# Kernel optimization log

Hardware: AMD Instinct MI355X
Metric: run time of the kernel (lower is better)

## Reference

```python
import jax, jax.numpy as jnp
import numpy as np

N, E, G = 100000, 800000, 4096
H, F_NODE, F_EDGE, T_OUT = 256, 133, 7, 12
NUM_LAYERS, NUM_TIMESTEPS = 4, 2
SLOPE = 0.01  # negative_slope used throughout AttentiveFP


def _lrelu(v):
    return jax.nn.leaky_relu(v, SLOPE)


def _seg_softmax(logits, seg, n):
    # PyG softmax: exp(x - segment_max) / (segment_sum + 1e-16)
    m = jax.ops.segment_max(logits, seg, num_segments=n)
    e = jnp.exp(logits - m[seg])
    s = jax.ops.segment_sum(e, seg, num_segments=n)
    return e / (s[seg] + 1e-16)


def _gru(xin, h, w_ih, w_hh, b_ih, b_hh):
    # torch.nn.GRUCell, gate order (r, z, n)
    gi = xin @ w_ih.T + b_ih
    gh = h @ w_hh.T + b_hh
    i_r, i_z, i_n = jnp.split(gi, 3, axis=-1)
    h_r, h_z, h_n = jnp.split(gh, 3, axis=-1)
    r = jax.nn.sigmoid(i_r + h_r)
    z = jax.nn.sigmoid(i_z + h_z)
    n = jnp.tanh(i_n + r * h_n)
    return (1.0 - z) * n + z * h


def setup_inputs() -> dict:
    key = jax.random.key(0)
    ks = iter(jax.random.split(key, 40))
    rn = lambda shape, s=0.1: jax.random.normal(next(ks), shape, jnp.float32) * s
    return {
        'x': jax.random.normal(next(ks), (N, F_NODE), jnp.float32),
        'edge_attr': jax.random.normal(next(ks), (E, F_EDGE), jnp.float32),
        'lin1_w': rn((H, F_NODE)), 'lin1_b': rn((H,)),
        'gate_att_l': rn((H,)), 'gate_att_r': rn((H,)),
        'gate_lin1_w': rn((H, H + F_EDGE)), 'gate_lin2_w': rn((H, H)), 'gate_bias': rn((H,)),
        'atom_lin_w': rn((NUM_LAYERS - 1, H, H)), 'atom_att_src': rn((NUM_LAYERS - 1, H)),
        'atom_att_dst': rn((NUM_LAYERS - 1, H)), 'atom_bias': rn((NUM_LAYERS - 1, H)),
        'gru_w_ih': rn((NUM_LAYERS, 3 * H, H)), 'gru_w_hh': rn((NUM_LAYERS, 3 * H, H)),
        'gru_b_ih': rn((NUM_LAYERS, 3 * H)), 'gru_b_hh': rn((NUM_LAYERS, 3 * H)),
        'mol_lin_w': rn((H, H)), 'mol_att_src': rn((H,)), 'mol_att_dst': rn((H,)), 'mol_bias': rn((H,)),
        'mol_gru_w_ih': rn((3 * H, H)), 'mol_gru_w_hh': rn((3 * H, H)),
        'mol_gru_b_ih': rn((3 * H,)), 'mol_gru_b_hh': rn((3 * H,)),
        'lin2_w': rn((H, H)), 'lin2_b': rn((H,)),
        'fc_w': rn((T_OUT, H)), 'fc_b': rn((T_OUT,)),
        'edge_index': jax.random.randint(next(ks), (2, E), 0, N),
        'batch': jnp.sort(jax.random.randint(next(ks), (N,), 0, G)),
        'num_graphs': G,
    }


def reference(x, edge_attr, lin1_w, lin1_b, gate_att_l, gate_att_r, gate_lin1_w,
              gate_lin2_w, gate_bias, atom_lin_w, atom_att_src, atom_att_dst, atom_bias,
              gru_w_ih, gru_w_hh, gru_b_ih, gru_b_hh, mol_lin_w, mol_att_src, mol_att_dst,
              mol_bias, mol_gru_w_ih, mol_gru_w_hh, mol_gru_b_ih, mol_gru_b_hh,
              lin2_w, lin2_b, fc_w, fc_b, edge_index, batch, num_graphs):
    # Eval mode: all dropouts are identity.
    src, dst = edge_index[0], edge_index[1]
    n = x.shape[0]

    x0 = _lrelu(x @ lin1_w.T + lin1_b)  # [N, H]

    # --- GATEConv: edge-feature attention message passing ---
    xj = _lrelu(jnp.concatenate([x0[src], edge_attr], axis=-1) @ gate_lin1_w.T)  # [E, H]
    alpha = _lrelu(xj @ gate_att_l + (x0 @ gate_att_r)[dst])
    alpha = _seg_softmax(alpha, dst, n)
    msg = (x0 @ gate_lin2_w.T)[src] * alpha[:, None]  # [E, H]
    h = jax.ops.segment_sum(msg, dst, num_segments=n) + gate_bias
    xcur = jax.nn.relu(_gru(jax.nn.elu(h), x0, gru_w_ih[0], gru_w_hh[0], gru_b_ih[0], gru_b_hh[0]))

    # --- (num_layers-1) GATConv layers (heads=1, no self loops, slope 0.01) ---
    for l in range(atom_lin_w.shape[0]):
        xl = xcur @ atom_lin_w[l].T  # [N, H]
        a = _lrelu((xl @ atom_att_src[l])[src] + (xl @ atom_att_dst[l])[dst])
        a = _seg_softmax(a, dst, n)
        h = jax.ops.segment_sum(xl[src] * a[:, None], dst, num_segments=n) + atom_bias[l]
        xcur = jax.nn.relu(_gru(jax.nn.elu(h), xcur,
                                gru_w_ih[l + 1], gru_w_hh[l + 1], gru_b_ih[l + 1], gru_b_hh[l + 1]))

    # --- Molecule embedding: attention pooling over node->graph bipartite edges ---
    out = jax.nn.relu(jax.ops.segment_sum(xcur, batch, num_segments=num_graphs))  # [G, H]
    xm = xcur @ mol_lin_w.T              # src transform, fixed across timesteps
    a_src = xm @ mol_att_src             # [N]
    for _ in range(NUM_TIMESTEPS):
        a = _lrelu(a_src + ((out @ mol_lin_w.T) @ mol_att_dst)[batch])
        a = _seg_softmax(a, batch, num_graphs)
        h = jax.ops.segment_sum(xm * a[:, None], batch, num_segments=num_graphs) + mol_bias
        out = jax.nn.relu(_gru(jax.nn.elu(h), out,
                               mol_gru_w_ih, mol_gru_w_hh, mol_gru_b_ih, mol_gru_b_hh))

    emb = out @ lin2_w.T + lin2_b        # AttentiveFP lin2
    return emb @ fc_w.T + fc_b           # [G, num_tasks]
```

## Files before the change

### kernel.cpp

```cpp
#include <hip/hip_runtime.h>
#include <math.h>
#include <stdio.h>
#include <stdint.h>

#define NH 256
#define NH3 768
#define FNODE 133
#define FEDGE 7
#define LDW_GATE1 263
#define NGRAPH 4096
#define NTASK 12
#define SLOPE 0.01f
#define CHUNK 25000
#define PADK 40
#define KPAD_X 160
#define LDC2 512
#define SCAN_TILE 2048

typedef __attribute__((ext_vector_type(4))) float f32x4;
typedef __attribute__((ext_vector_type(8))) _Float16 f16x8;
typedef __attribute__((ext_vector_type(4))) _Float16 f16x4;
typedef __attribute__((ext_vector_type(2))) _Float16 f16x2;

static __device__ __forceinline__ float lrelu_f(float x) { return x > 0.f ? x : SLOPE * x; }
static __device__ __forceinline__ f16x2 lrelu2(f16x2 v) {
    f16x2 z = {(_Float16)0.f, (_Float16)0.f};
    f16x2 s = {(_Float16)SLOPE, (_Float16)SLOPE};
    return __builtin_elementwise_max(v, z) + __builtin_elementwise_min(v, z) * s;
}

template<int ACT>
static __device__ __forceinline__ void gemm16_core(
    _Float16* As, _Float16* Ws,
    const _Float16* __restrict__ A, const _Float16* __restrict__ Wf,
    const float* __restrict__ bias, const float* __restrict__ bias2,
    _Float16* __restrict__ Cout,
    int M, int K, int ldA, int ldC, int ocol)
{
    const int bm = blockIdx.y * 64;
    const int tid = threadIdx.x;
    const int wv = tid >> 6, lane = tid & 63;
    const int l15 = lane & 15, l4 = lane >> 4;
    const int ar = tid >> 2, akq = (tid & 3) * 8;
    const int ga = bm + ar;

    f16x8 ra, rw[4];
    auto loadT = [&](int k0) {
        if (ga < M) ra = *reinterpret_cast<const f16x8*>(A + (size_t)ga * ldA + k0 + akq);
        else { f16x8 z = {}; ra = z; }
#pragma unroll
        for (int q = 0; q < 4; ++q)
            rw[q] = *reinterpret_cast<const f16x8*>(Wf + (size_t)(ar + 64 * q) * K + k0 + akq);
    };

    f32x4 acc[16];
#pragma unroll
    for (int c = 0; c < 16; ++c) acc[c] = (f32x4){0.f, 0.f, 0.f, 0.f};

    loadT(0);
    for (int k0 = 0; k0 < K; k0 += 32) {
        *reinterpret_cast<f16x8*>(&As[ar * PADK + akq]) = ra;
#pragma unroll
        for (int q = 0; q < 4; ++q)
            *reinterpret_cast<f16x8*>(&Ws[(ar + 64 * q) * PADK + akq]) = rw[q];
        __syncthreads();
        if (k0 + 32 < K) loadT(k0 + 32);
        f16x8 af = *reinterpret_cast<const f16x8*>(&As[(wv * 16 + l15) * PADK + l4 * 8]);
#pragma unroll
        for (int c = 0; c < 16; ++c) {
            f16x8 wf = *reinterpret_cast<const f16x8*>(&Ws[(c * 16 + l15) * PADK + l4 * 8]);
            acc[c] = __builtin_amdgcn_mfma_f32_16x16x32_f16(af, wf, acc[c], 0, 0, 0);
        }
        __syncthreads();
    }

#pragma unroll
    for (int c = 0; c < 16; ++c) {
        int gc = c * 16 + l15;
        float bv = (bias ? bias[gc] : 0.f) + (bias2 ? bias2[gc] : 0.f);
#pragma unroll
        for (int q = 0; q < 4; ++q) {
            int gr = bm + wv * 16 + l4 * 4 + q;
            if (gr >= M) continue;
            float v = acc[c][q] + bv;
            if (ACT == 1) v = lrelu_f(v);
            else if (ACT == 2) v = (v > 0.f ? v : expm1f(v));
            else if (ACT == 3) v = 1.f / (1.f + expf(-v));
            Cout[(size_t)gr * ldC + ocol + gc] = (_Float16)v;
        }
    }
}

template<int ACT>
__global__ __launch_bounds__(256, 4) void gemm16(
    const _Float16* __restrict__ A, const _Float16* __restrict__ Wf,
    const float* __restrict__ bias, _Float16* __restrict__ Cout,
    int M, int K, int ldA, int ldC, int ocol)
{
    __shared__ _Float16 As[64 * PADK];
    __shared__ _Float16 Ws[256 * PADK];
    gemm16_core<ACT>(As, Ws, A, Wf, bias, nullptr, Cout, M, K, ldA, ldC, ocol);
}

__global__ __launch_bounds__(256, 4) void gemm_gru_a16(
    const _Float16* __restrict__ Acat, const _Float16* __restrict__ wcat16,
    const _Float16* __restrict__ wihn16,
    const float* __restrict__ bih, const float* __restrict__ bhh,
    _Float16* __restrict__ srz, _Float16* __restrict__ innb, int mc)
{
    __shared__ _Float16 As[64 * PADK];
    __shared__ _Float16 Ws[256 * PADK];
    int z = blockIdx.z;
    if (z < 2)
        gemm16_core<3>(As, Ws, Acat, wcat16 + (size_t)z * 256 * 512, bih + z * 256, bhh + z * 256,
                       srz, mc, 512, LDC2, 512, z * 256);
    else
        gemm16_core<0>(As, Ws, Acat, wihn16, bih + 512, nullptr, innb, mc, 256, LDC2, 256, 0);
}

__global__ __launch_bounds__(256, 4) void gemm_gru_b16(
    _Float16* __restrict__ Acat, const _Float16* __restrict__ Wn16, const float* __restrict__ bhh,
    const _Float16* __restrict__ srz, const _Float16* __restrict__ innb,
    const float* __restrict__ us, const float* __restrict__ ud,
    float* __restrict__ dotr, float* __restrict__ adst, int mc)
{
    __shared__ _Float16 As[64 * PADK];
    __shared__ _Float16 Ws[256 * PADK];
    const int bm = blockIdx.y * 64;
    const int tid = threadIdx.x;
    const int wv = tid >> 6, lane = tid & 63;
    const int l15 = lane & 15, l4 = lane >> 4;
    const int ar = tid >> 2, akq = (tid & 3) * 8;
    const int ga = bm + ar;

    f16x8 ra, rw[4];
    auto loadT = [&](int k0) {
        if (ga < mc) ra = *reinterpret_cast<const f16x8*>(Acat + (size_t)ga * LDC2 + NH + k0 + akq);
        else { f16x8 z = {}; ra = z; }
#pragma unroll
        for (int q = 0; q < 4; ++q)
            rw[q] = *reinterpret_cast<const f16x8*>(Wn16 + (size_t)(ar + 64 * q) * NH + k0 + akq);
    };

    f32x4 acc[16];
#pragma unroll
    for (int c = 0; c < 16; ++c) acc[c] = (f32x4){0.f, 0.f, 0.f, 0.f};

    loadT(0);
    for (int k0 = 0; k0 < NH; k0 += 32) {
        *reinterpret_cast<f16x8*>(&As[ar * PADK + akq]) = ra;
#pragma unroll
        for (int q = 0; q < 4; ++q)
            *reinterpret_cast<f16x8*>(&Ws[(ar + 64 * q) * PADK + akq]) = rw[q];
        __syncthreads();
        if (k0 + 32 < NH) loadT(k0 + 32);
        f16x8 af = *reinterpret_cast<const f16x8*>(&As[(wv * 16 + l15) * PADK + l4 * 8]);
#pragma unroll
        for (int c = 0; c < 16; ++c) {
            f16x8 wf = *reinterpret_cast<const f16x8*>(&Ws[(c * 16 + l15) * PADK + l4 * 8]);
            acc[c] = __builtin_amdgcn_mfma_f32_16x16x32_f16(af, wf, acc[c], 0, 0, 0);
        }
        __syncthreads();
    }

    float pd1[4] = {0.f, 0.f, 0.f, 0.f};
    float pd2[4] = {0.f, 0.f, 0.f, 0.f};
#pragma unroll
    for (int c = 0; c < 16; ++c) {
        int gc = c * 16 + l15;
        float bhn = bhh[512 + gc];
        float usv = us ? us[gc] : 0.f;
        float udv = ud ? ud[gc] : 0.f;
#pragma unroll
        for (int q = 0; q < 4; ++q) {
            int gr = bm + wv * 16 + l4 * 4 + q;
            if (gr >= mc) continue;
            float hn = acc[c][q] + bhn;
            float rr = (float)srz[(size_t)gr * 512 + gc];
            float zz = (float)srz[(size_t)gr * 512 + 256 + gc];
            float inn = (float)innb[(size_t)gr * NH + gc];
            float nn = tanhf(inn + rr * hn);
            size_t xoff = (size_t)gr * LDC2 + NH + gc;
            float xold = (float)Acat[xoff];
            float hv = fmaxf((1.f - zz) * nn + zz * xold, 0.f);
            Acat[xoff] = (_Float16)hv;
            pd1[q] += hv * usv;
            pd2[q] += hv * udv;
        }
    }
    if (us) {
#pragma unroll
        for (int off = 1; off < 16; off <<= 1) {
#pragma unroll
            for (int q = 0; q < 4; ++q) {
                pd1[q] += __shfl_xor(pd1[q], off);
                pd2[q] += __shfl_xor(pd2[q], off);
            }
        }
        if (l15 == 0) {
#pragma unroll
            for (int q = 0; q < 4; ++q) {
                int gr = bm + wv * 16 + l4 * 4 + q;
                if (gr < mc) {
                    dotr[gr] = pd1[q];
                    if (ud) adst[gr] = pd2[q];
                }
            }
        }
    }
}

template<int ACT, int OB, int AF16>
static __device__ __forceinline__ void gemm_core(
    _Float16* As, _Float16* Ws,
    const void* __restrict__ Av, const float* __restrict__ W,
    const float* __restrict__ bias, void* __restrict__ Cout,
    int M, int K, int Nout, int ldA, int ldW, int ldC, int ocol, int Kw, int bn)
{
    const int bm = blockIdx.y * 64;
    const int tid = threadIdx.x;
    const int wv = tid >> 6, lane = tid & 63;
    const int l15 = lane & 15, l4 = lane >> 4;
    const bool kvec = ((K & 31) == 0) && ((ldA & 3) == 0);
    const bool wvec = ((K & 31) == 0) && ((ldW & 3) == 0) && (Kw == K);
    const int ar = tid >> 2, akq = (tid & 3) * 8;

    f32x4 acc[16];
#pragma unroll
    for (int c = 0; c < 16; ++c) acc[c] = (f32x4){0.f, 0.f, 0.f, 0.f};

    for (int k0 = 0; k0 < K; k0 += 32) {
        {
            const int ga = bm + ar;
            _Float16* dstA = &As[ar * PADK + akq];
            if (AF16) {
                const _Float16* A = (const _Float16*)Av;
                if (ga < M) {
                    *reinterpret_cast<f16x8*>(dstA) =
                        *reinterpret_cast<const f16x8*>(A + (size_t)ga * ldA + k0 + akq);
                } else {
#pragma unroll
                    for (int j = 0; j < 8; ++j) dstA[j] = (_Float16)0.f;
                }
            } else {
                const float* A = (const float*)Av;
                if (ga < M && kvec) {
                    const float4* ap4 = reinterpret_cast<const float4*>(A + (size_t)ga * ldA + k0 + akq);
                    float4 v0 = ap4[0], v1 = ap4[1];
                    dstA[0] = (_Float16)v0.x; dstA[1] = (_Float16)v0.y;
                    dstA[2] = (_Float16)v0.z; dstA[3] = (_Float16)v0.w;
                    dstA[4] = (_Float16)v1.x; dstA[5] = (_Float16)v1.y;
                    dstA[6] = (_Float16)v1.z; dstA[7] = (_Float16)v1.w;
                } else {
                    const float* ap = A + (size_t)ga * ldA + k0 + akq;
#pragma unroll
                    for (int j = 0; j < 8; ++j) {
                        int gk = k0 + akq + j;
                        float v = (ga < M && gk < K) ? ap[j] : 0.f;
                        dstA[j] = (_Float16)v;
                    }
                }
            }
        }
#pragma unroll
        for (int q = 0; q < 4; ++q) {
            const int r = ar + 64 * q;
            const int gw = bn + r;
            _Float16* dstW = &Ws[r * PADK + akq];
            if (gw < Nout && wvec) {
                const float4* wp4 = reinterpret_cast<const float4*>(W + (size_t)gw * ldW + k0 + akq);
                float4 v0 = wp4[0], v1 = wp4[1];
                dstW[0] = (_Float16)v0.x; dstW[1] = (_Float16)v0.y;
                dstW[2] = (_Float16)v0.z; dstW[3] = (_Float16)v0.w;
                dstW[4] = (_Float16)v1.x; dstW[5] = (_Float16)v1.y;
                dstW[6] = (_Float16)v1.z; dstW[7] = (_Float16)v1.w;
            } else {
                const float* wp = W + (size_t)gw * ldW + k0 + akq;
#pragma unroll
                for (int j = 0; j < 8; ++j) {
                    int gk = k0 + akq + j;
                    float v = (gw < Nout && gk < Kw) ? wp[j] : 0.f;
                    dstW[j] = (_Float16)v;
                }
            }
        }
        __syncthreads();
        f16x8 af = *reinterpret_cast<const f16x8*>(&As[(wv * 16 + l15) * PADK + l4 * 8]);
#pragma unroll
        for (int c = 0; c < 16; ++c) {
            f16x8 wf = *reinterpret_cast<const f16x8*>(&Ws[(c * 16 + l15) * PADK + l4 * 8]);
            acc[c] = __builtin_amdgcn_mfma_f32_16x16x32_f16(af, wf, acc[c], 0, 0, 0);
        }
        __syncthreads();
    }

#pragma unroll
    for (int c = 0; c < 16; ++c) {
        int gc = bn + c * 16 + l15;
        if (gc >= Nout) continue;
        float bv = bias ? bias[gc] : 0.f;
#pragma unroll
        for (int q = 0; q < 4; ++q) {
            int gr = bm + wv * 16 + l4 * 4 + q;
            if (gr >= M) continue;
            float v = acc[c][q] + bv;
            if (ACT == 1) v = lrelu_f(v);
            else if (ACT == 2) v = (v > 0.f ? v : expm1f(v));
            size_t off = (size_t)gr * ldC + ocol + gc;
            if (OB) ((_Float16*)Cout)[off] = (_Float16)v;
            else    ((float*)Cout)[off] = v;
        }
    }
}

template<int ACT, int OB, int AF16>
__global__ __launch_bounds__(256, 4) void gemm_mfma(
    const void* __restrict__ A, const float* __restrict__ W,
    const float* __restrict__ bias, void* __restrict__ Cout,
    int M, int K, int Nout, int ldA, int ldW, int ldC, int ocol, int Kw)
{
    __shared__ _Float16 As[64 * PADK];
    __shared__ _Float16 Ws[256 * PADK];
    gemm_core<ACT, OB, AF16>(As, Ws, A, W, bias, Cout, M, K, Nout, ldA, ldW, ldC, ocol, Kw,
                             blockIdx.x * 256);
}

template<int ACT, int OB>
__global__ __launch_bounds__(256, 4) void gemm_mfma2(
    const float* __restrict__ A0, const float* __restrict__ A1,
    const float* __restrict__ W0, const float* __restrict__ W1,
    void* __restrict__ C0, void* __restrict__ C1, int M, int K, int Nout)
{
    __shared__ _Float16 As[64 * PADK];
    __shared__ _Float16 Ws[256 * PADK];
    int bn = blockIdx.x * 256;
    if (blockIdx.z == 0)
        gemm_core<ACT, OB, 0>(As, Ws, A0, W0, nullptr, C0, M, K, Nout, K, K, Nout, 0, K, bn);
    else
        gemm_core<ACT, OB, 0>(As, Ws, A1, W1, nullptr, C1, M, K, Nout, K, K, Nout, 0, K, bn);
}

__global__ void cast_w16(const float* __restrict__ src, _Float16* __restrict__ dst,
                         int rows, int cols, int ldsrc, int kout)
{
    int i = blockIdx.x * 256 + threadIdx.x;
    if (i >= rows * kout) return;
    int r = i / kout, k = i % kout;
    dst[i] = (k < cols) ? (_Float16)src[(size_t)r * ldsrc + k] : (_Float16)0.f;
}
__global__ void build_wcat16(const float* __restrict__ wih, const float* __restrict__ whh,
                             _Float16* __restrict__ dst)
{
    int i = blockIdx.x * 256 + threadIdx.x;
    if (i >= 512 * 512) return;
    int j = i >> 9, k = i & 511;
    dst[i] = (_Float16)((k < 256) ? wih[j * 256 + k] : whh[j * 256 + (k - 256)]);
}

__global__ void pad_cast_f16(const float* __restrict__ in, _Float16* __restrict__ out,
                             int M, int Kin, int Kout)
{
    size_t i = (size_t)blockIdx.x * 256 + threadIdx.x;
    if (i >= (size_t)M * Kout) return;
    int r = (int)(i / Kout), k = (int)(i % Kout);
    out[i] = (k < Kin) ? (_Float16)in[(size_t)r * Kin + k] : (_Float16)0.f;
}

__global__ __launch_bounds__(256) void gemm_nt(
    const float* __restrict__ A, const float* __restrict__ W,
    const float* __restrict__ bias, float* __restrict__ C,
    int M, int K, int Nout, int ldW, int act)
{
    __shared__ float As[16][65];
    __shared__ float Ws[16][65];
    const int bm = blockIdx.y * 64;
    const int bn = blockIdx.x * 64;
    const int tid = threadIdx.x;
    const int tr = tid >> 4, tc = tid & 15;
    const int lrow = tid >> 2, lk = (tid & 3) * 4;
    float acc[4][4] = {};
    for (int k0 = 0; k0 < K; k0 += 16) {
#pragma unroll
        for (int j = 0; j < 4; ++j) {
            int gk = k0 + lk + j;
            int ga = bm + lrow;
            As[lk + j][lrow] = (ga < M && gk < K) ? A[(size_t)ga * K + gk] : 0.f;
            int gw = bn + lrow;
            Ws[lk + j][lrow] = (gw < Nout && gk < K) ? W[(size_t)gw * ldW + gk] : 0.f;
        }
        __syncthreads();
#pragma unroll
        for (int kk = 0; kk < 16; ++kk) {
            float av[4], bv[4];
#pragma unroll
            for (int i = 0; i < 4; ++i) av[i] = As[kk][tr * 4 + i];
#pragma unroll
            for (int i = 0; i < 4; ++i) bv[i] = Ws[kk][tc * 4 + i];
#pragma unroll
            for (int i = 0; i < 4; ++i)
#pragma unroll
                for (int j = 0; j < 4; ++j) acc[i][j] += av[i] * bv[j];
        }
        __syncthreads();
    }
#pragma unroll
    for (int i = 0; i < 4; ++i) {
        int m = bm + tr * 4 + i;
        if (m >= M) continue;
#pragma unroll
        for (int j = 0; j < 4; ++j) {
            int n = bn + tc * 4 + j;
            if (n >= Nout) continue;
            float v = acc[i][j];
            if (bias) v += bias[n];
            if (act == 1) v = lrelu_f(v);
            C[(size_t)m * Nout + n] = v;
        }
    }
}

__global__ void zero_i32(int* p, int n) {
    int i = blockIdx.x * 256 + threadIdx.x;
    if (i < n) p[i] = 0;
}
__global__ void hist_k(const int* __restrict__ key, int* __restrict__ deg, int E) {
    int i = blockIdx.x * 256 + threadIdx.x;
    if (i < E) atomicAdd(&deg[key[i]], 1);
}
__global__ __launch_bounds__(256) void scan_pass1(
    const int* __restrict__ deg, int* __restrict__ bsum, int Nn)
{
    __shared__ int lds[256];
    int b = blockIdx.x, t = threadIdx.x;
    int base = b * SCAN_TILE + t * 8;
    int s = 0;
#pragma unroll
    for (int q = 0; q < 8; ++q) { int i = base + q; if (i < Nn) s += deg[i]; }
    lds[t] = s;
    __syncthreads();
    for (int off = 128; off; off >>= 1) {
        if (t < off) lds[t] += lds[t + off];
        __syncthreads();
    }
    if (t == 0) bsum[b] = lds[0];
}
__global__ __launch_bounds__(256) void scan_pass2(
    const int* __restrict__ bsum, int* __restrict__ boff, int nb, int* __restrict__ total)
{
    __shared__ int lds[256];
    int t = threadIdx.x;
    int v = (t < nb) ? bsum[t] : 0;
    lds[t] = v;
    __syncthreads();
    for (int off = 1; off < 256; off <<= 1) {
        int u = (t >= off) ? lds[t - off] : 0;
        __syncthreads();
        lds[t] += u;
        __syncthreads();
    }
    if (t < nb) boff[t] = lds[t] - v;
    if (t == 255 && total) *total = lds[255];
}
__global__ __launch_bounds__(256) void scan_pass3(
    const int* __restrict__ deg, const int* __restrict__ boff,
    int* __restrict__ rowptr, int* __restrict__ cursor, int Nn)
{
    __shared__ int lds[256];
    int b = blockIdx.x, t = threadIdx.x;
    int base = b * SCAN_TILE + t * 8;
    int v[8];
    int s = 0;
#pragma unroll
    for (int q = 0; q < 8; ++q) { int i = base + q; v[q] = (i < Nn) ? deg[i] : 0; s += v[q]; }
    lds[t] = s;
    __syncthreads();
    for (int off = 1; off < 256; off <<= 1) {
        int u = (t >= off) ? lds[t - off] : 0;
        __syncthreads();
        lds[t] += u;
        __syncthreads();
    }
    int run = boff[b] + lds[t] - s;
#pragma unroll
    for (int q = 0; q < 8; ++q) {
        int i = base + q;
        if (i < Nn) { rowptr[i] = run; cursor[i] = run; run += v[q]; }
    }
}
__global__ void csr_scatter(const int* __restrict__ src, const int* __restrict__ dst,
                            int* __restrict__ cursor, int* __restrict__ esrc,
                            int* __restrict__ pos, int E)
{
    int e = blockIdx.x * 256 + threadIdx.x;
    if (e < E) {
        int p = atomicAdd(&cursor[dst[e]], 1);
        esrc[p] = src[e];
        pos[e] = p;
    }
}
__global__ void csc_scatter(const int* __restrict__ src, int* __restrict__ cursor,
                            int* __restrict__ seid, int E)
{
    int e = blockIdx.x * 256 + threadIdx.x;
    if (e < E) {
        int p = atomicAdd(&cursor[src[e]], 1);
        seid[p] = e;
    }
}
__global__ void edge_csc_build(const float* __restrict__ edge_attr, const int* __restrict__ seid,
                               const int* __restrict__ pos, _Float16* __restrict__ ecsc,
                               int* __restrict__ pcsc, int E)
{
    int p = blockIdx.x * 256 + threadIdx.x;
    if (p >= E) return;
    int e = seid[p];
    pcsc[p] = pos[e];
    const float* ep = edge_attr + (size_t)e * FEDGE;
#pragma unroll
    for (int f = 0; f < FEDGE; ++f) ecsc[(size_t)p * 8 + f] = (_Float16)ep[f];
    ecsc[(size_t)p * 8 + 7] = (_Float16)0.f;
}
__global__ void gptr_build(const int* __restrict__ batch, int* __restrict__ gptr, int Nn, int G) {
    int g = blockIdx.x * 256 + threadIdx.x;
    if (g > G) return;
    int lo = 0, hi = Nn;
    while (lo < hi) { int mid = (lo + hi) >> 1; if (batch[mid] < g) lo = mid + 1; else hi = mid; }
    gptr[g] = lo;
}

__global__ __launch_bounds__(256) void gate_part_csc(
    const _Float16* __restrict__ nodepart, const _Float16* __restrict__ ecsc,
    const float* __restrict__ gate_lin1_w, const float* __restrict__ att_l,
    const int* __restrict__ srowptr, const int* __restrict__ pcsc,
    float* __restrict__ elogp, int Nn)
{
    int wv = threadIdx.x >> 6, lane = threadIdx.x & 63;
    int h0 = lane * 4;
    f16x2 wr2[2][FEDGE], al2[2];
#pragma unroll
    for (int p = 0; p < 2; ++p) {
        int ha = h0 + 2 * p, hb = ha + 1;
#pragma unroll
        for (int f = 0; f < FEDGE; ++f) {
            wr2[p][f][0] = (_Float16)gate_lin1_w[(size_t)ha * LDW_GATE1 + NH + f];
            wr2[p][f][1] = (_Float16)gate_lin1_w[(size_t)hb * LDW_GATE1 + NH + f];
        }
        al2[p][0] = (_Float16)att_l[ha];
        al2[p][1] = (_Float16)att_l[hb];
    }
    for (int s = blockIdx.x * 4 + wv; s < Nn; s += gridDim.x * 4) {
        int beg = srowptr[s], end = srowptr[s + 1];
        if (beg >= end) continue;
        f16x4 np4 = *reinterpret_cast<const f16x4*>(nodepart + (size_t)s * NH + h0);
        f16x2 np2[2];
        np2[0][0] = np4[0]; np2[0][1] = np4[1];
        np2[1][0] = np4[2]; np2[1][1] = np4[3];
        for (int j0 = beg; j0 < end; j0 += 4) {
            int nb = end - j0; if (nb > 4) nb = 4;
            f16x8 ev[4];
            int pp[4];
#pragma unroll
            for (int k = 0; k < 4; ++k) {
                int j = (k < nb) ? j0 + k : beg;
                pp[k] = pcsc[j];
                ev[k] = *reinterpret_cast<const f16x8*>(ecsc + (size_t)j * 8);
            }
            float acc[4];
#pragma unroll
            for (int k = 0; k < 4; ++k) {
                f16x2 v0 = np2[0], v1 = np2[1];
#pragma unroll
                for (int f = 0; f < FEDGE; ++f) {
                    f16x2 e2; e2[0] = ev[k][f]; e2[1] = ev[k][f];
                    v0 += e2 * wr2[0][f];
                    v1 += e2 * wr2[1][f];
                }
                float a = __builtin_amdgcn_fdot2(lrelu2(v0), al2[0], 0.f, false);
                a = __builtin_amdgcn_fdot2(lrelu2(v1), al2[1], a, false);
                acc[k] = a;
            }
#pragma unroll
            for (int off = 32; off; off >>= 1) {
#pragma unroll
                for (int k = 0; k < 4; ++k) acc[k] += __shfl_xor(acc[k], off);
            }
            if (lane == 0) {
#pragma unroll
                for (int k = 0; k < 4; ++k) if (k < nb) elogp[pp[k]] = acc[k];
            }
        }
    }
}

__global__ __launch_bounds__(256) void gat_agg_csr(
    const _Float16* __restrict__ X, int ldX,
    const float* __restrict__ asrc, const float* __restrict__ adst,
    const int* __restrict__ rowptr, const int* __restrict__ esrc,
    _Float16* __restrict__ hout, int Nn)
{
    __shared__ float salpha[4][64];
    int wv = threadIdx.x >> 6, lane = threadIdx.x & 63;
    int d = blockIdx.x * 4 + wv;
    if (d >= Nn) return;
    int beg = rowptr[d], end = rowptr[d + 1];
    float a0 = 0.f, a1 = 0.f, a2 = 0.f, a3 = 0.f, ssum = 0.f;
    if (beg < end) {
        float ad = adst[d];
        float m = -3.4e38f;
        for (int j = beg + lane; j < end; j += 64)
            m = fmaxf(m, lrelu_f(asrc[esrc[j]] + ad));
#pragma unroll
        for (int off = 32; off; off >>= 1) m = fmaxf(m, __shfl_xor(m, off));
        for (int c0 = beg; c0 < end; c0 += 64) {
            int j = c0 + lane;
            float e = (j < end) ? expf(lrelu_f(asrc[esrc[j]] + ad) - m) : 0.f;
            salpha[wv][lane] = e;
            ssum += e;
            int cend = end - c0; if (cend > 64) cend = 64;
            for (int k = 0; k < cend; ++k) {
                float alk = salpha[wv][k];
                int sj = esrc[c0 + k];
                f16x4 xv = *reinterpret_cast<const f16x4*>(X + (size_t)sj * ldX + lane * 4);
                a0 += alk * (float)xv[0]; a1 += alk * (float)xv[1];
                a2 += alk * (float)xv[2]; a3 += alk * (float)xv[3];
            }
        }
#pragma unroll
        for (int off = 32; off; off >>= 1) ssum += __shfl_xor(ssum, off);
        float inv = 1.f / (ssum + 1e-16f);
        a0 *= inv; a1 *= inv; a2 *= inv; a3 *= inv;
    }
    f16x4 o;
    o[0] = (_Float16)a0; o[1] = (_Float16)a1; o[2] = (_Float16)a2; o[3] = (_Float16)a3;
    *reinterpret_cast<f16x4*>(hout + (size_t)d * NH + lane * 4) = o;
}

__global__ __launch_bounds__(256) void gate_agg_csr(
    const _Float16* __restrict__ X, int ldX,
    const float* __restrict__ elogp, const float* __restrict__ dotr,
    const int* __restrict__ rowptr, const int* __restrict__ esrc,
    _Float16* __restrict__ hout, int Nn)
{
    __shared__ float salpha[4][64];
    int wv = threadIdx.x >> 6, lane = threadIdx.x & 63;
    int d = blockIdx.x * 4 + wv;
    if (d >= Nn) return;
    int beg = rowptr[d], end = rowptr[d + 1];
    float a0 = 0.f, a1 = 0.f, a2 = 0.f, a3 = 0.f, ssum = 0.f;
    if (beg < end) {
        float dd = dotr[d];
        float m = -3.4e38f;
        for (int j = beg + lane; j < end; j += 64)
            m = fmaxf(m, lrelu_f(elogp[j] + dd));
#pragma unroll
        for (int off = 32; off; off >>= 1) m = fmaxf(m, __shfl_xor(m, off));
        for (int c0 = beg; c0 < end; c0 += 64) {
            int j = c0 + lane;
            float e = (j < end) ? expf(lrelu_f(elogp[j] + dd) - m) : 0.f;
            salpha[wv][lane] = e;
            ssum += e;
            int cend = end - c0; if (cend > 64) cend = 64;
            for (int k = 0; k < cend; ++k) {
                float alk = salpha[wv][k];
                int sj = esrc[c0 + k];
                f16x4 xv = *reinterpret_cast<const f16x4*>(X + (size_t)sj * ldX + lane * 4);
                a0 += alk * (float)xv[0]; a1 += alk * (float)xv[1];
                a2 += alk * (float)xv[2]; a3 += alk * (float)xv[3];
            }
        }
#pragma unroll
        for (int off = 32; off; off >>= 1) ssum += __shfl_xor(ssum, off);
        float inv = 1.f / (ssum + 1e-16f);
        a0 *= inv; a1 *= inv; a2 *= inv; a3 *= inv;
    }
    f16x4 o;
    o[0] = (_Float16)a0; o[1] = (_Float16)a1; o[2] = (_Float16)a2; o[3] = (_Float16)a3;
    *reinterpret_cast<f16x4*>(hout + (size_t)d * NH + lane * 4) = o;
}

__global__ __launch_bounds__(256) void mol_agg_csr(
    const _Float16* __restrict__ X, int ldX,
    const float* __restrict__ dotr, const float* __restrict__ ddot,
    const int* __restrict__ gptr, float* __restrict__ hout, int G)
{
    __shared__ float salpha[4][64];
    int wv = threadIdx.x >> 6, lane = threadIdx.x & 63;
    int g = blockIdx.x * 4 + wv;
    if (g >= G) return;
    int beg = gptr[g], end = gptr[g + 1];
    float a0 = 0.f, a1 = 0.f, a2 = 0.f, a3 = 0.f, ssum = 0.f;
    if (beg < end) {
        float dg = ddot[g];
        float m = -3.4e38f;
        for (int i = beg + lane; i < end; i += 64)
            m = fmaxf(m, lrelu_f(dotr[i] + dg));
#pragma unroll
        for (int off = 32; off; off >>= 1) m = fmaxf(m, __shfl_xor(m, off));
        for (int c0 = beg; c0 < end; c0 += 64) {
            int i = c0 + lane;
            float e = (i < end) ? expf(lrelu_f(dotr[i] + dg) - m) : 0.f;
            salpha[wv][lane] = e;
            ssum += e;
            int cend = end - c0; if (cend > 64) cend = 64;
            for (int k = 0; k < cend; ++k) {
                float alk = salpha[wv][k];
                f16x4 xv = *reinterpret_cast<const f16x4*>(X + (size_t)(c0 + k) * ldX + lane * 4);
                a0 += alk * (float)xv[0]; a1 += alk * (float)xv[1];
                a2 += alk * (float)xv[2]; a3 += alk * (float)xv[3];
            }
        }
#pragma unroll
        for (int off = 32; off; off >>= 1) ssum += __shfl_xor(ssum, off);
        float inv = 1.f / (ssum + 1e-16f);
        a0 *= inv; a1 *= inv; a2 *= inv; a3 *= inv;
    }
    float* hr = hout + (size_t)g * NH + lane * 4;
    hr[0] = a0; hr[1] = a1; hr[2] = a2; hr[3] = a3;
}

__global__ __launch_bounds__(256) void graph_sum_relu(
    const _Float16* __restrict__ X, int ldX, const int* __restrict__ gptr,
    float* __restrict__ out, int G)
{
    int wv = threadIdx.x >> 6, lane = threadIdx.x & 63;
    int g = blockIdx.x * 4 + wv;
    if (g >= G) return;
    int beg = gptr[g], end = gptr[g + 1];
    float a0 = 0.f, a1 = 0.f, a2 = 0.f, a3 = 0.f;
    for (int i = beg; i < end; ++i) {
        f16x4 xv = *reinterpret_cast<const f16x4*>(X + (size_t)i * ldX + lane * 4);
        a0 += (float)xv[0]; a1 += (float)xv[1]; a2 += (float)xv[2]; a3 += (float)xv[3];
    }
    float* hr = out + (size_t)g * NH + lane * 4;
    hr[0] = fmaxf(a0, 0.f); hr[1] = fmaxf(a1, 0.f);
    hr[2] = fmaxf(a2, 0.f); hr[3] = fmaxf(a3, 0.f);
}

template<typename TX>
__global__ __launch_bounds__(256) void node_dot(
    const TX* __restrict__ X, int ldX, const float* __restrict__ v1, const float* __restrict__ v2,
    float* __restrict__ o1, float* __restrict__ o2, int M)
{
    __shared__ float s1[NH], s2[NH];
    int tid = threadIdx.x;
    s1[tid] = v1[tid];
    s2[tid] = v2 ? v2[tid] : 0.f;
    __syncthreads();
    int wv = tid >> 6, lane = tid & 63;
    for (int n = blockIdx.x * 4 + wv; n < M; n += gridDim.x * 4) {
        float a1 = 0.f, a2 = 0.f;
#pragma unroll
        for (int i = 0; i < 4; ++i) {
            int hh = i * 64 + lane;
            float xv = (float)X[(size_t)n * ldX + hh];
            a1 += xv * s1[hh];
            a2 += xv * s2[hh];
        }
#pragma unroll
        for (int off = 32; off; off >>= 1) { a1 += __shfl_xor(a1, off); a2 += __shfl_xor(a2, off); }
        if (lane == 0) { o1[n] = a1; if (o2) o2[n] = a2; }
    }
}

__global__ __launch_bounds__(256) void matvec_left(
    const float* __restrict__ Wm, const float* __restrict__ a, float* __restrict__ v)
{
    int j = threadIdx.x;
    float s = 0.f;
    for (int i = 0; i < NH; ++i) s += a[i] * Wm[(size_t)i * NH + j];
    v[j] = s;
}

__global__ __launch_bounds__(256) void gru_combine(
    const _Float16* __restrict__ gi, const _Float16* __restrict__ gh,
    const float* __restrict__ b_ih, const float* __restrict__ b_hh,
    const float* __restrict__ hprev, float* __restrict__ out, int M)
{
    size_t t = (size_t)blockIdx.x * 256 + threadIdx.x;
    if (t >= (size_t)M * 32) return;
    int n = (int)(t >> 5), j0 = ((int)t & 31) * 8;
    size_t b3 = (size_t)n * NH3;
    f16x8 vir = *reinterpret_cast<const f16x8*>(&gi[b3 + j0]);
    f16x8 viz = *reinterpret_cast<const f16x8*>(&gi[b3 + NH + j0]);
    f16x8 vin = *reinterpret_cast<const f16x8*>(&gi[b3 + 2 * NH + j0]);
    f16x8 vhr = *reinterpret_cast<const f16x8*>(&gh[b3 + j0]);
    f16x8 vhz = *reinterpret_cast<const f16x8*>(&gh[b3 + NH + j0]);
    f16x8 vhn = *reinterpret_cast<const f16x8*>(&gh[b3 + 2 * NH + j0]);
    size_t hb = (size_t)n * NH + j0;
#pragma unroll
    for (int q = 0; q < 8; ++q) {
        int j = j0 + q;
        float r = 1.f / (1.f + expf(-((float)vir[q] + b_ih[j] + (float)vhr[q] + b_hh[j])));
        float z = 1.f / (1.f + expf(-((float)viz[q] + b_ih[NH + j] + (float)vhz[q] + b_hh[NH + j])));
        float nn = tanhf((float)vin[q] + b_ih[2 * NH + j] + r * ((float)vhn[q] + b_hh[2 * NH + j]));
        out[hb + q] = fmaxf((1.f - z) * nn + z * hprev[hb + q], 0.f);
    }
}

extern "C" void kernel_launch(void* const* d_in, const int* in_sizes, int n_in,
                              void* d_out, int out_size, void* d_ws, size_t ws_size,
                              hipStream_t stream)
{
    const float* x          = (const float*)d_in[0];
    const float* edge_attr  = (const float*)d_in[1];
    const float* lin1_w     = (const float*)d_in[2];
    const float* lin1_b     = (const float*)d_in[3];
    const float* gate_att_l = (const float*)d_in[4];
    const float* gate_att_r = (const float*)d_in[5];
    const float* gate_lin1_w= (const float*)d_in[6];
    const float* gate_lin2_w= (const float*)d_in[7];
    const float* gate_bias  = (const float*)d_in[8];
    const float* atom_lin_w = (const float*)d_in[9];
    const float* atom_att_src=(const float*)d_in[10];
    const float* atom_att_dst=(const float*)d_in[11];
    const float* atom_bias  = (const float*)d_in[12];
    const float* gru_w_ih   = (const float*)d_in[13];
    const float* gru_w_hh   = (const float*)d_in[14];
    const float* gru_b_ih   = (const float*)d_in[15];
    const float* gru_b_hh   = (const float*)d_in[16];
    const float* mol_lin_w  = (const float*)d_in[17];
    const float* mol_att_src= (const float*)d_in[18];
    const float* mol_att_dst= (const float*)d_in[19];
    const float* mol_bias   = (const float*)d_in[20];
    const float* mol_gru_w_ih=(const float*)d_in[21];
    const float* mol_gru_w_hh=(const float*)d_in[22];
    const float* mol_gru_b_ih=(const float*)d_in[23];
    const float* mol_gru_b_hh=(const float*)d_in[24];
    const float* lin2_w     = (const float*)d_in[25];
    const float* lin2_b     = (const float*)d_in[26];
    const float* fc_w       = (const float*)d_in[27];
    const float* fc_b       = (const float*)d_in[28];
    const int*   edge_index = (const int*)d_in[29];
    const int*   batch      = (const int*)d_in[30];

    const int N = in_sizes[0] / FNODE;
    const int E = in_sizes[1] / FEDGE;
    const int G = NGRAPH;
    const int* src = edge_index;
    const int* dst = edge_index + E;

    float* w = (float*)d_ws;
    size_t o = 0;
    auto alloc = [&](size_t cnt) { size_t r = o; o += cnt; return r; };
    const size_t o_B1cat = alloc((size_t)N * NH);
    const size_t o_B2    = alloc((size_t)N * NH / 2);
    const size_t o_B3    = alloc((size_t)CHUNK * 512);
    const size_t o_w16   = alloc((size_t)972000);
    const size_t o_elog  = alloc((size_t)E);
    const size_t o_dotr  = alloc((size_t)N);
    const size_t o_adst  = alloc((size_t)N);
    const size_t o_ddot  = alloc((size_t)G);
    const size_t o_vvec  = alloc((size_t)NH);
    const size_t o_usrc  = alloc((size_t)NH);
    const size_t o_udst  = alloc((size_t)NH);
    const size_t o_rowp  = alloc((size_t)N + 1);
    const size_t o_srowp = alloc((size_t)N + 1);
    const size_t o_deg   = alloc((size_t)N);
    const size_t o_curs  = alloc((size_t)N);
    const size_t o_bsum  = alloc((size_t)512);
    const size_t o_esrc  = alloc((size_t)E);
    const size_t o_pos   = alloc((size_t)E);
    const size_t o_seid  = alloc((size_t)E);
    const size_t o_ecsc  = alloc((size_t)E * 4);
    const size_t o_pcsc  = alloc((size_t)E);
    const size_t o_gptr  = alloc((size_t)G + 1);
    if (o * sizeof(float) > ws_size) {
        fprintf(stderr, "kernel_launch: ws too small: need %zu have %zu\n", o * 4, ws_size);
        return;
    }

    _Float16* B1cat = (_Float16*)(w + o_B1cat);
    _Float16* xcur  = B1cat + NH;
    _Float16* B2 = (_Float16*)(w + o_B2);
    float* B3   = w + o_B3;
    _Float16* w16 = (_Float16*)(w + o_w16);
    _Float16* lin116   = w16;
    _Float16* gate1a16 = lin116 + 40960;
    _Float16* gate216  = gate1a16 + 65536;
    _Float16* atom16   = gate216 + 65536;
    _Float16* wihn16   = atom16 + 3 * 65536;
    _Float16* whhn16   = wihn16 + 4 * 65536;
    _Float16* wcat16   = whhn16 + 4 * 65536;
    float* elog = w + o_elog;
    float* dotr = w + o_dotr;
    float* adst = w + o_adst;
    float* ddot = w + o_ddot;
    float* vvec = w + o_vvec;
    float* usrc = w + o_usrc;
    float* udst = w + o_udst;
    int* rowptr  = (int*)(w + o_rowp);
    int* srowptr = (int*)(w + o_srowp);
    int* deg     = (int*)(w + o_deg);
    int* cursor  = (int*)(w + o_curs);
    int* bsum    = (int*)(w + o_bsum);
    int* boff    = bsum + 256;
    int* esrc    = (int*)(w + o_esrc);
    int* pos     = (int*)(w + o_pos);
    int* seid    = (int*)(w + o_seid);
    _Float16* ecsc = (_Float16*)(w + o_ecsc);
    int* pcsc    = (int*)(w + o_pcsc);
    int* gptr    = (int*)(w + o_gptr);

    float* B2f = (float*)B2;
    float*    gout   = B2f;
    float*    hraw_g = B2f + (size_t)G * NH;
    float*    h_g    = B2f + (size_t)2 * G * NH;
    _Float16* gig    = (_Float16*)(B2f + (size_t)3 * G * NH);
    _Float16* ghg    = (_Float16*)(B2f + (size_t)3 * G * NH + (size_t)G * NH3 / 2);
    float*    emb    = B2f + (size_t)3 * G * NH + (size_t)G * NH3;

    const int BLK = 256;
    auto cdiv = [](size_t a, size_t b) { return (int)((a + b - 1) / b); };
    const int gridNodeWave = cdiv(N, 4);
    const int gridEdgeThr = cdiv(E, BLK);
    const int gridNodeThr = cdiv(N, BLK);
    const int CAP = 4096;
    const int gridNodeCap = gridNodeWave < CAP ? gridNodeWave : CAP;
    const int nScanB = cdiv(N, SCAN_TILE);

    auto run_scan = [&](int* rowp) {
        scan_pass1<<<nScanB, BLK, 0, stream>>>(deg, bsum, N);
        scan_pass2<<<1, BLK, 0, stream>>>(bsum, boff, nScanB, rowp + N);
        scan_pass3<<<nScanB, BLK, 0, stream>>>(deg, boff, rowp, cursor, N);
    };

    cast_w16<<<cdiv(256 * 160, BLK), BLK, 0, stream>>>(lin1_w, lin116, 256, FNODE, FNODE, 160);
    cast_w16<<<cdiv(65536, BLK), BLK, 0, stream>>>(gate_lin1_w, gate1a16, 256, 256, LDW_GATE1, 256);
    cast_w16<<<cdiv(65536, BLK), BLK, 0, stream>>>(gate_lin2_w, gate216, 256, 256, 256, 256);
    for (int l = 0; l < 3; ++l)
        cast_w16<<<cdiv(65536, BLK), BLK, 0, stream>>>(atom_lin_w + (size_t)l * 65536,
                                                       atom16 + (size_t)l * 65536, 256, 256, 256, 256);
    for (int l = 0; l < 4; ++l) {
        const float* wih = gru_w_ih + (size_t)l * NH3 * NH;
        const float* whh = gru_w_hh + (size_t)l * NH3 * NH;
        build_wcat16<<<1024, BLK, 0, stream>>>(wih, whh, wcat16 + (size_t)l * 262144);
        cast_w16<<<cdiv(65536, BLK), BLK, 0, stream>>>(wih + 512 * NH, wihn16 + (size_t)l * 65536,
                                                       256, 256, 256, 256);
        cast_w16<<<cdiv(65536, BLK), BLK, 0, stream>>>(whh + 512 * NH, whhn16 + (size_t)l * 65536,
                                                       256, 256, 256, 256);
    }

    zero_i32<<<gridNodeThr, BLK, 0, stream>>>(deg, N);
    hist_k<<<gridEdgeThr, BLK, 0, stream>>>(dst, deg, E);
    run_scan(rowptr);
    csr_scatter<<<gridEdgeThr, BLK, 0, stream>>>(src, dst, cursor, esrc, pos, E);
    zero_i32<<<gridNodeThr, BLK, 0, stream>>>(deg, N);
    hist_k<<<gridEdgeThr, BLK, 0, stream>>>(src, deg, E);
    run_scan(srowptr);
    csc_scatter<<<gridEdgeThr, BLK, 0, stream>>>(src, cursor, seid, E);
    edge_csc_build<<<gridEdgeThr, BLK, 0, stream>>>(edge_attr, seid, pos, ecsc, pcsc, E);
    gptr_build<<<cdiv(G + 1, BLK), BLK, 0, stream>>>(batch, gptr, N, G);

    auto run_tail = [&](const _Float16* Wh16, const float* bh, int l,
                        const float* bih, const float* bhh,
                        const float* usv, const float* udv) {
        _Float16* innb = (_Float16*)B3;
        _Float16* srz  = innb + (size_t)CHUNK * NH;
        dim3 gFull(1, cdiv(N, 64));
        gemm16<2><<<gFull, BLK, 0, stream>>>(B2, Wh16, bh, B1cat, N, NH, NH, LDC2, 0);
        for (int c0 = 0; c0 < N; c0 += CHUNK) {
            int mc = (N - c0) < CHUNK ? (N - c0) : CHUNK;
            dim3 gA(1, cdiv(mc, 64), 3);
            gemm_gru_a16<<<gA, BLK, 0, stream>>>(B1cat + (size_t)c0 * LDC2,
                                                 wcat16 + (size_t)l * 262144,
                                                 wihn16 + (size_t)l * 65536,
                                                 bih, bhh, srz, innb, mc);
            dim3 gB(1, cdiv(mc, 64));
            gemm_gru_b16<<<gB, BLK, 0, stream>>>(B1cat + (size_t)c0 * LDC2,
                                                 whhn16 + (size_t)l * 65536, bhh,
                                                 srz, innb, usv, udv, dotr + c0, adst + c0, mc);
        }
    };

    dim3 gridNH(1, cdiv(N, 64));

    _Float16* xpad = (_Float16*)B3;
    pad_cast_f16<<<cdiv((size_t)N * KPAD_X, BLK), BLK, 0, stream>>>(x, xpad, N, FNODE, KPAD_X);
    gemm16<1><<<gridNH, BLK, 0, stream>>>(xpad, lin116, lin1_b, B1cat, N, KPAD_X, KPAD_X, LDC2, NH);

    gemm16<0><<<gridNH, BLK, 0, stream>>>(xcur, gate1a16, nullptr, B2, N, NH, LDC2, NH, 0);
    node_dot<_Float16><<<gridNodeCap, BLK, 0, stream>>>(xcur, LDC2, gate_att_r, nullptr,
                                                        dotr, nullptr, N);
    gate_part_csc<<<gridNodeCap, BLK, 0, stream>>>(B2, ecsc, gate_lin1_w, gate_att_l,
                                                   srowptr, pcsc, elog, N);
    gate_agg_csr<<<gridNodeWave, BLK, 0, stream>>>(xcur, LDC2, elog, dotr, rowptr, esrc, B2, N);
    matvec_left<<<1, BLK, 0, stream>>>(atom_lin_w, atom_att_src, usrc);
    matvec_left<<<1, BLK, 0, stream>>>(atom_lin_w, atom_att_dst, udst);
    run_tail(gate216, gate_bias, 0, gru_b_ih, gru_b_hh, usrc, udst);

    for (int l = 0; l < 3; ++l) {
        gat_agg_csr<<<gridNodeWave, BLK, 0, stream>>>(xcur, LDC2, dotr, adst, rowptr, esrc, B2, N);
        const float* nus = usrc;
        const float* nud = udst;
        if (l < 2) {
            matvec_left<<<1, BLK, 0, stream>>>(atom_lin_w + (size_t)(l + 1) * NH * NH,
                                               atom_att_src + (l + 1) * NH, usrc);
            matvec_left<<<1, BLK, 0, stream>>>(atom_lin_w + (size_t)(l + 1) * NH * NH,
                                               atom_att_dst + (l + 1) * NH, udst);
        } else {
            matvec_left<<<1, BLK, 0, stream>>>(mol_lin_w, mol_att_src, usrc);
            nud = nullptr;
        }
        run_tail(atom16 + (size_t)l * 65536, atom_bias + l * NH, l + 1,
                 gru_b_ih + (size_t)(l + 1) * NH3, gru_b_hh + (size_t)(l + 1) * NH3, nus, nud);
    }

    const int gridGWave = cdiv(G, 4);
    graph_sum_relu<<<gridGWave, BLK, 0, stream>>>(xcur, LDC2, gptr, gout, G);
    matvec_left<<<1, BLK, 0, stream>>>(mol_lin_w, mol_att_dst, vvec);

    dim3 gridGH(1, cdiv(G, 64));
    dim3 gridGD(3, cdiv(G, 64), 2);
    for (int t = 0; t < 2; ++t) {
        node_dot<float><<<gridGWave, BLK, 0, stream>>>(gout, NH, vvec, nullptr, ddot, nullptr, G);
        mol_agg_csr<<<gridGWave, BLK, 0, stream>>>(xcur, LDC2, dotr, ddot, gptr, hraw_g, G);
        gemm_mfma<2, 0, 0><<<gridGH, BLK, 0, stream>>>(hraw_g, mol_lin_w, mol_bias, h_g,
                                                       G, NH, NH, NH, NH, NH, 0, NH);
        gemm_mfma2<0, 1><<<gridGD, BLK, 0, stream>>>(h_g, gout, mol_gru_w_ih, mol_gru_w_hh,
                                                     gig, ghg, G, NH, NH3);
        gru_combine<<<cdiv((size_t)G * 32, BLK), BLK, 0, stream>>>(
            gig, ghg, mol_gru_b_ih, mol_gru_b_hh, gout, gout, G);
    }

    gemm_mfma<0, 0, 0><<<gridGH, BLK, 0, stream>>>(gout, lin2_w, lin2_b, emb,
                                                   G, NH, NH, NH, NH, NH, 0, NH);
    dim3 gridFc(1, cdiv(G, 64));
    gemm_nt<<<gridFc, BLK, 0, stream>>>(emb, fc_w, fc_b, (float*)d_out, G, NH, NTASK, NH, 0);
}
```

Baseline: 2.805 ms.

## Fuse GRU r/z gate GEMMs into 512-wide tile and double-buffer register prefetch

The r and z gate GEMMs are merged into one kernel that computes a 64x512 tile, so each A tile is loaded once for both gates instead of being re-read by separate blocks. The generic GEMM core gets a two-stage register prefetch, unrolled by two k-steps. CHUNK rises to 34000, so fewer chunk iterations are needed, and the B3 workspace is resized to match. The fused kernel needs 32 accumulator vectors and twice the weight LDS, and launch bounds are lowered, which reduces occupancy.

```diff
diff --git a/kernel.cpp b/kernel.cpp
--- a/kernel.cpp
+++ b/kernel.cpp
@@ -11,7 +11,7 @@
 #define NGRAPH 4096
 #define NTASK 12
 #define SLOPE 0.01f
-#define CHUNK 25000
+#define CHUNK 34000
 #define PADK 40
 #define KPAD_X 160
 #define LDC2 512
@@ -44,33 +44,65 @@
     const int ar = tid >> 2, akq = (tid & 3) * 8;
     const int ga = bm + ar;
 
-    f16x8 ra, rw[4];
-    auto loadT = [&](int k0) {
-        if (ga < M) ra = *reinterpret_cast<const f16x8*>(A + (size_t)ga * ldA + k0 + akq);
-        else { f16x8 z = {}; ra = z; }
-#pragma unroll
-        for (int q = 0; q < 4; ++q)
-            rw[q] = *reinterpret_cast<const f16x8*>(Wf + (size_t)(ar + 64 * q) * K + k0 + akq);
+    f16x8 a0, w00, w01, w02, w03;
+    f16x8 a1, w10, w11, w12, w13;
+    auto load0 = [&](int k0) {
+        if (ga < M) a0 = *reinterpret_cast<const f16x8*>(A + (size_t)ga * ldA + k0 + akq);
+        else { f16x8 z = {}; a0 = z; }
+        w00 = *reinterpret_cast<const f16x8*>(Wf + (size_t)ar * K + k0 + akq);
+        w01 = *reinterpret_cast<const f16x8*>(Wf + (size_t)(ar + 64) * K + k0 + akq);
+        w02 = *reinterpret_cast<const f16x8*>(Wf + (size_t)(ar + 128) * K + k0 + akq);
+        w03 = *reinterpret_cast<const f16x8*>(Wf + (size_t)(ar + 192) * K + k0 + akq);
     };
+    auto load1 = [&](int k0) {
+        if (ga < M) a1 = *reinterpret_cast<const f16x8*>(A + (size_t)ga * ldA + k0 + akq);
+        else { f16x8 z = {}; a1 = z; }
+        w10 = *reinterpret_cast<const f16x8*>(Wf + (size_t)ar * K + k0 + akq);
+        w11 = *reinterpret_cast<const f16x8*>(Wf + (size_t)(ar + 64) * K + k0 + akq);
+        w12 = *reinterpret_cast<const f16x8*>(Wf + (size_t)(ar + 128) * K + k0 + akq);
+        w13 = *reinterpret_cast<const f16x8*>(Wf + (size_t)(ar + 192) * K + k0 + akq);
+    };
+    auto stage0 = [&]() {
+        *reinterpret_cast<f16x8*>(&As[ar * PADK + akq]) = a0;
+        *reinterpret_cast<f16x8*>(&Ws[ar * PADK + akq]) = w00;
+        *reinterpret_cast<f16x8*>(&Ws[(ar + 64) * PADK + akq]) = w01;
+        *reinterpret_cast<f16x8*>(&Ws[(ar + 128) * PADK + akq]) = w02;
+        *reinterpret_cast<f16x8*>(&Ws[(ar + 192) * PADK + akq]) = w03;
+    };
+    auto stage1 = [&]() {
+        *reinterpret_cast<f16x8*>(&As[ar * PADK + akq]) = a1;
+        *reinterpret_cast<f16x8*>(&Ws[ar * PADK + akq]) = w10;
+        *reinterpret_cast<f16x8*>(&Ws[(ar + 64) * PADK + akq]) = w11;
+        *reinterpret_cast<f16x8*>(&Ws[(ar + 128) * PADK + akq]) = w12;
+        *reinterpret_cast<f16x8*>(&Ws[(ar + 192) * PADK + akq]) = w13;
+    };
 
     f32x4 acc[16];
 #pragma unroll
     for (int c = 0; c < 16; ++c) acc[c] = (f32x4){0.f, 0.f, 0.f, 0.f};
 
-    loadT(0);
-    for (int k0 = 0; k0 < K; k0 += 32) {
-        *reinterpret_cast<f16x8*>(&As[ar * PADK + akq]) = ra;
-#pragma unroll
-        for (int q = 0; q < 4; ++q)
-            *reinterpret_cast<f16x8*>(&Ws[(ar + 64 * q) * PADK + akq]) = rw[q];
-        __syncthreads();
-        if (k0 + 32 < K) loadT(k0 + 32);
+    auto mmac = [&]() {
         f16x8 af = *reinterpret_cast<const f16x8*>(&As[(wv * 16 + l15) * PADK + l4 * 8]);
 #pragma unroll
         for (int c = 0; c < 16; ++c) {
             f16x8 wf = *reinterpret_cast<const f16x8*>(&Ws[(c * 16 + l15) * PADK + l4 * 8]);
             acc[c] = __builtin_amdgcn_mfma_f32_16x16x32_f16(af, wf, acc[c], 0, 0, 0);
         }
+    };
+
+    load0(0);
+    if (K > 32) load1(32);
+    for (int k0 = 0; k0 < K; k0 += 64) {
+        stage0();
+        __syncthreads();
+        if (k0 + 64 < K) load0(k0 + 64);
+        mmac();
+        __syncthreads();
+        if (k0 + 32 >= K) break;
+        stage1();
+        __syncthreads();
+        if (k0 + 96 < K) load1(k0 + 96);
+        mmac();
         __syncthreads();
     }
 
@@ -92,7 +124,7 @@
 }
 
 template<int ACT>
-__global__ __launch_bounds__(256, 4) void gemm16(
+__global__ __launch_bounds__(256, 3) void gemm16(
     const _Float16* __restrict__ A, const _Float16* __restrict__ Wf,
     const float* __restrict__ bias, _Float16* __restrict__ Cout,
     int M, int K, int ldA, int ldC, int ocol)
@@ -102,20 +134,67 @@
     gemm16_core<ACT>(As, Ws, A, Wf, bias, nullptr, Cout, M, K, ldA, ldC, ocol);
 }
 
-__global__ __launch_bounds__(256, 4) void gemm_gru_a16(
+__global__ __launch_bounds__(256, 2) void gemm_gru_rzi16(
     const _Float16* __restrict__ Acat, const _Float16* __restrict__ wcat16,
     const _Float16* __restrict__ wihn16,
     const float* __restrict__ bih, const float* __restrict__ bhh,
     _Float16* __restrict__ srz, _Float16* __restrict__ innb, int mc)
 {
     __shared__ _Float16 As[64 * PADK];
-    __shared__ _Float16 Ws[256 * PADK];
-    int z = blockIdx.z;
-    if (z < 2)
-        gemm16_core<3>(As, Ws, Acat, wcat16 + (size_t)z * 256 * 512, bih + z * 256, bhh + z * 256,
-                       srz, mc, 512, LDC2, 512, z * 256);
-    else
+    __shared__ _Float16 Ws[512 * PADK];
+    if (blockIdx.z == 1) {
         gemm16_core<0>(As, Ws, Acat, wihn16, bih + 512, nullptr, innb, mc, 256, LDC2, 256, 0);
+        return;
+    }
+    const int bm = blockIdx.y * 64;
+    const int tid = threadIdx.x;
+    const int wv = tid >> 6, lane = tid & 63;
+    const int l15 = lane & 15, l4 = lane >> 4;
+    const int ar = tid >> 2, akq = (tid & 3) * 8;
+    const int ga = bm + ar;
+
+    f16x8 ra, rw[8];
+    auto loadT = [&](int k0) {
+        if (ga < mc) ra = *reinterpret_cast<const f16x8*>(Acat + (size_t)ga * LDC2 + k0 + akq);
+        else { f16x8 z = {}; ra = z; }
+#pragma unroll
+        for (int q = 0; q < 8; ++q)
+            rw[q] = *reinterpret_cast<const f16x8*>(wcat16 + (size_t)(ar + 64 * q) * 512 + k0 + akq);
+    };
+
+    f32x4 acc[32];
+#pragma unroll
+    for (int c = 0; c < 32; ++c) acc[c] = (f32x4){0.f, 0.f, 0.f, 0.f};
+
+    loadT(0);
+    for (int k0 = 0; k0 < 512; k0 += 32) {
+        *reinterpret_cast<f16x8*>(&As[ar * PADK + akq]) = ra;
+#pragma unroll
+        for (int q = 0; q < 8; ++q)
+            *reinterpret_cast<f16x8*>(&Ws[(ar + 64 * q) * PADK + akq]) = rw[q];
+        __syncthreads();
+        if (k0 + 32 < 512) loadT(k0 + 32);
+        f16x8 af = *reinterpret_cast<const f16x8*>(&As[(wv * 16 + l15) * PADK + l4 * 8]);
+#pragma unroll
+        for (int c = 0; c < 32; ++c) {
+            f16x8 wf = *reinterpret_cast<const f16x8*>(&Ws[(c * 16 + l15) * PADK + l4 * 8]);
+            acc[c] = __builtin_amdgcn_mfma_f32_16x16x32_f16(af, wf, acc[c], 0, 0, 0);
+        }
+        __syncthreads();
+    }
+
+#pragma unroll
+    for (int c = 0; c < 32; ++c) {
+        int gc = c * 16 + l15;
+        float bv = bih[gc] + bhh[gc];
+#pragma unroll
+        for (int q = 0; q < 4; ++q) {
+            int gr = bm + wv * 16 + l4 * 4 + q;
+            if (gr >= mc) continue;
+            float v = 1.f / (1.f + expf(-(acc[c][q] + bv)));
+            srz[(size_t)gr * 512 + gc] = (_Float16)v;
+        }
+    }
 }
 
 __global__ __launch_bounds__(256, 4) void gemm_gru_b16(
@@ -844,7 +923,7 @@
     auto alloc = [&](size_t cnt) { size_t r = o; o += cnt; return r; };
     const size_t o_B1cat = alloc((size_t)N * NH);
     const size_t o_B2    = alloc((size_t)N * NH / 2);
-    const size_t o_B3    = alloc((size_t)CHUNK * 512);
+    const size_t o_B3    = alloc((size_t)CHUNK * 384);
     const size_t o_w16   = alloc((size_t)972000);
     const size_t o_elog  = alloc((size_t)E);
     const size_t o_dotr  = alloc((size_t)N);
@@ -960,11 +1039,11 @@
         gemm16<2><<<gFull, BLK, 0, stream>>>(B2, Wh16, bh, B1cat, N, NH, NH, LDC2, 0);
         for (int c0 = 0; c0 < N; c0 += CHUNK) {
             int mc = (N - c0) < CHUNK ? (N - c0) : CHUNK;
-            dim3 gA(1, cdiv(mc, 64), 3);
-            gemm_gru_a16<<<gA, BLK, 0, stream>>>(B1cat + (size_t)c0 * LDC2,
-                                                 wcat16 + (size_t)l * 262144,
-                                                 wihn16 + (size_t)l * 65536,
-                                                 bih, bhh, srz, innb, mc);
+            dim3 gA(1, cdiv(mc, 64), 2);
+            gemm_gru_rzi16<<<gA, BLK, 0, stream>>>(B1cat + (size_t)c0 * LDC2,
+                                                   wcat16 + (size_t)l * 262144,
+                                                   wihn16 + (size_t)l * 65536,
+                                                   bih, bhh, srz, innb, mc);
             dim3 gB(1, cdiv(mc, 64));
             gemm_gru_b16<<<gB, BLK, 0, stream>>>(B1cat + (size_t)c0 * LDC2,
                                                  whhn16 + (size_t)l * 65536, bhh,
```

Result: slower. 3.332 ms (+18.8%).
